# Performance work log

Hardware: AMD Instinct MI355X
Metric: run time of the kernel (lower is better)

## Reference

```python
import jax, jax.numpy as jnp
import numpy as np

B, T, D, H = 4, 2048, 512, 8
DH = D // H  # 64

def setup_inputs() -> dict:
    key = jax.random.key(0)
    kx, kq, kk, kv = jax.random.split(key, 4)
    s = 0.02
    return {
        "x": jax.random.normal(kx, (B, T, D), dtype=jnp.float32),
        "Wq": jax.random.normal(kq, (D, D), dtype=jnp.float32) * s,
        "Wk": jax.random.normal(kk, (D, D), dtype=jnp.float32) * s,
        "Wv": jax.random.normal(kv, (D, D), dtype=jnp.float32) * s,
    }

def reference(x, Wq, Wk, Wv):
    b, t, _ = x.shape
    # nn.Linear(bias=False): y = x @ W.T
    q = (x @ Wq.T).reshape(b, t, H, DH).transpose(0, 2, 1, 3)  # (B,H,T,DH)
    k = (x @ Wk.T).reshape(b, t, H, DH).transpose(0, 2, 1, 3)
    v = (x @ Wv.T).reshape(b, t, H, DH).transpose(0, 2, 1, 3)
    scale = 1.0 / jnp.sqrt(jnp.float32(DH))
    att = jnp.einsum('bhqd,bhkd->bhqk', q, k) * scale  # (B,H,T,T)
    causal = jnp.tril(jnp.ones((t, t), dtype=bool))
    att = jnp.where(causal, att, jnp.float32(-jnp.inf))
    att = jax.nn.softmax(att, axis=-1)
    out = jnp.einsum('bhqk,bhkd->bhqd', att, v)  # (B,H,T,DH)
    return out.transpose(0, 2, 1, 3).reshape(b, t, D)
```

## Files before the change

### kernel.cpp

```cpp
#include <hip/hip_runtime.h>
#include <math.h>

#define B_ 4
#define T_ 2048
#define D_ 512
#define H_ 8
#define DH_ 64

typedef __attribute__((ext_vector_type(8))) short bf16x8;
typedef __attribute__((ext_vector_type(4))) float f32x4;

__device__ inline unsigned short f2b(float x) {
    unsigned int u = __float_as_uint(x);
    return (unsigned short)((u + 0x7FFFu + ((u >> 16) & 1u)) >> 16);
}

__global__ __launch_bounds__(256) void cvt_kernel(
    const float* __restrict__ x,  const float* __restrict__ wq,
    const float* __restrict__ wk, const float* __restrict__ wv,
    unsigned short* __restrict__ xb,  unsigned short* __restrict__ wqb,
    unsigned short* __restrict__ wkb, unsigned short* __restrict__ wvb)
{
    const int bid = blockIdx.x;
    const float* src;
    unsigned short* dst;
    size_t base;
    if (bid < 4096) { src = x; dst = xb; base = (size_t)bid * 1024; }
    else {
        const int s  = (bid - 4096) >> 8;
        const int lb = (bid - 4096) & 255;
        src = (s == 0) ? wq : (s == 1) ? wk : wv;
        dst = (s == 0) ? wqb : (s == 1) ? wkb : wvb;
        base = (size_t)lb * 1024;
    }
    const size_t idx = base + (size_t)threadIdx.x * 4;
    float4 f = *(const float4*)(src + idx);
    ushort4 r;
    r.x = f2b(f.x); r.y = f2b(f.y); r.z = f2b(f.z); r.w = f2b(f.w);
    *(ushort4*)(dst + idx) = r;
}

__global__ __launch_bounds__(256) void qkv_mfma_kernel(
    const unsigned short* __restrict__ xb,
    const unsigned short* __restrict__ wqb,
    const unsigned short* __restrict__ wkb,
    const unsigned short* __restrict__ wvb,
    unsigned short* __restrict__ Qo,
    unsigned short* __restrict__ Ko,
    unsigned short* __restrict__ Vto)
{
    const int z = blockIdx.z;
    const unsigned short* Ap;
    const unsigned short* Bp;
    int m0, n0;
    if (z < 2) {
        Ap = xb; Bp = (z == 0) ? wqb : wkb;
        m0 = blockIdx.x * 128;
        n0 = blockIdx.y * 128;
    } else {
        Ap = wvb; Bp = xb;
        m0 = blockIdx.y * 128;
        n0 = blockIdx.x * 128;
    }
    const int tid = threadIdx.x;
    const int w   = tid >> 6;
    const int l   = tid & 63;
    const int l15 = l & 15;
    const int lg  = l >> 4;
    const int wm  = (w >> 1) * 64;
    const int wn  = (w & 1) * 64;

    __shared__ __align__(16) char lds[32768];
    char* As = lds;
    char* Bs = lds + 16384;

    f32x4 acc[4][4];
    #pragma unroll
    for (int i = 0; i < 4; ++i)
        #pragma unroll
        for (int j = 0; j < 4; ++j) acc[i][j] = (f32x4){0.f, 0.f, 0.f, 0.f};

    bf16x8 areg[4], breg[4];

    #define QLOAD(KS) {                                                        \
        _Pragma("unroll")                                                      \
        for (int i_ = 0; i_ < 4; ++i_) {                                       \
            const int q_ = tid + 256 * i_, r_ = q_ >> 3, c_ = q_ & 7;          \
            areg[i_] = *(const bf16x8*)(Ap + (size_t)(m0 + r_) * 512 + (KS) * 64 + c_ * 8); \
            breg[i_] = *(const bf16x8*)(Bp + (size_t)(n0 + r_) * 512 + (KS) * 64 + c_ * 8); \
        } }

    QLOAD(0);

    for (int ks = 0; ks < 8; ++ks) {
        __syncthreads();
        #pragma unroll
        for (int i = 0; i < 4; ++i) {
            const int q = tid + 256 * i, r = q >> 3, c = q & 7;
            const int off = r * 128 + ((c ^ (r & 7)) << 4);
            *(bf16x8*)(As + off) = areg[i];
            *(bf16x8*)(Bs + off) = breg[i];
        }
        __syncthreads();

        if (ks < 7) QLOAD(ks + 1);

        bf16x8 af[4][2], bf[4][2];
        #pragma unroll
        for (int im = 0; im < 4; ++im) {
            const int r = wm + im * 16 + l15;
            const int rb = r * 128, sw = r & 7;
            af[im][0] = *(const bf16x8*)(As + rb + ((lg ^ sw) << 4));
            af[im][1] = *(const bf16x8*)(As + rb + (((4 + lg) ^ sw) << 4));
        }
        #pragma unroll
        for (int jn = 0; jn < 4; ++jn) {
            const int r = wn + jn * 16 + l15;
            const int rb = r * 128, sw = r & 7;
            bf[jn][0] = *(const bf16x8*)(Bs + rb + ((lg ^ sw) << 4));
            bf[jn][1] = *(const bf16x8*)(Bs + rb + (((4 + lg) ^ sw) << 4));
        }
        #pragma unroll
        for (int im = 0; im < 4; ++im)
            #pragma unroll
            for (int jn = 0; jn < 4; ++jn) {
                acc[im][jn] = __builtin_amdgcn_mfma_f32_16x16x32_bf16(
                    af[im][0], bf[jn][0], acc[im][jn], 0, 0, 0);
                acc[im][jn] = __builtin_amdgcn_mfma_f32_16x16x32_bf16(
                    af[im][1], bf[jn][1], acc[im][jn], 0, 0, 0);
            }
    }

    #undef QLOAD

    if (z < 2) {
        unsigned short* Y = (z == 0) ? Qo : Ko;
        #pragma unroll
        for (int im = 0; im < 4; ++im)
            #pragma unroll
            for (int jn = 0; jn < 4; ++jn)
                #pragma unroll
                for (int r4 = 0; r4 < 4; ++r4) {
                    const int row = m0 + wm + im * 16 + lg * 4 + r4;
                    const int col = n0 + wn + jn * 16 + l15;
                    Y[(size_t)row * 512 + col] = f2b(acc[im][jn][r4]);
                }
    } else {
        #pragma unroll
        for (int im = 0; im < 4; ++im)
            #pragma unroll
            for (int jn = 0; jn < 4; ++jn)
                #pragma unroll
                for (int r4 = 0; r4 < 4; ++r4) {
                    const int rowW = m0 + wm + im * 16 + lg * 4 + r4;
                    const int ct   = n0 + wn + jn * 16 + l15;
                    const int b    = ct >> 11;
                    const int tl   = ct & 2047;
                    Vto[((size_t)(b * 512 + rowW)) * 2048 + tl] = f2b(acc[im][jn][r4]);
                }
    }
}

__global__ __launch_bounds__(256) void attn_mfma_kernel(
    const unsigned short* __restrict__ Q,
    const unsigned short* __restrict__ K,
    const unsigned short* __restrict__ Vt,
    float* __restrict__ O)
{
    const int bid = blockIdx.x;
    const int g   = bid & 31;
    const int h   = g & 7;
    const int b   = g >> 3;
    const int qi  = bid >> 5;
    const int qk_ = qi >> 3, qq_ = qi & 7;
    const int qt  = (qk_ == 0) ? 31 - qq_
                  : (qk_ == 1) ? qq_
                  : (qk_ == 2) ? 23 - qq_
                  :              8 + qq_;
    const int nkt = qt + 1;
    const int tid = threadIdx.x;
    const int w   = tid >> 6;
    const int l   = tid & 63;
    const int l15 = l & 15;
    const int lg  = l >> 4;

    __shared__ __align__(16) char lds[40960];
    char* pw = lds + 32768 + w * 2048;

    const float C  = 0.18033688011112042f;
    const float MC = 32.0f * C;

    const int c0   = tid;
    const int c1   = tid + 256;
    const int row0 = c0 >> 3, seg0 = c0 & 7;
    const int row1 = c1 >> 3, seg1 = c1 & 7;
    const int off0 = row0 * 128 + ((seg0 * 16) ^ ((row0 & 7) << 4));
    const int off1 = row1 * 128 + ((seg1 * 16) ^ ((row1 & 7) << 4));

    const int rowV  = tid >> 2, sp = tid & 3;
    const int kA    = (sp & 1) * 8 + (sp & 2) * 16;
    const int vswz  = (rowV & 7) << 4;
    const int voff0 = rowV * 128 + ((sp * 32) ^ vswz);
    const int voff1 = rowV * 128 + ((sp * 32 + 16) ^ vswz);

    const int t_q      = qt * 64 + w * 16 + l15;
    const size_t qbase = ((size_t)(b * T_ + t_q)) * D_ + h * DH_ + lg * 8;
    const bf16x8 qf0 = *(const bf16x8*)(Q + qbase);
    const bf16x8 qf1 = *(const bf16x8*)(Q + qbase + 32);

    const unsigned short* Ksrc0 = K + ((size_t)(b * T_ + row0)) * D_ + h * DH_ + seg0 * 8;
    const unsigned short* Ksrc1 = K + ((size_t)(b * T_ + row1)) * D_ + h * DH_ + seg1 * 8;
    const unsigned short* VsrcA = Vt + ((size_t)b * D_ + h * DH_ + rowV) * T_ + kA;

    f32x4 o[4];
    #pragma unroll
    for (int d = 0; d < 4; ++d) o[d] = (f32x4){0.f, 0.f, 0.f, 0.f};
    float lrow[4] = {0.f, 0.f, 0.f, 0.f};

    bf16x8 kc0, kc1;
    uint4 va, vb4;

    #define LOADT(KT) {                                                   \
        kc0 = *(const bf16x8*)(Ksrc0 + (size_t)(KT) * (64 * D_));         \
        kc1 = *(const bf16x8*)(Ksrc1 + (size_t)(KT) * (64 * D_));         \
        va  = *(const uint4*)(VsrcA + (KT) * 64);                         \
        vb4 = *(const uint4*)(VsrcA + (KT) * 64 + 16);                    \
    }
    #define WRITEBUF(BI) {                                                \
        char* dK_ = lds + (BI) * 16384;                                   \
        char* dV_ = dK_ + 8192;                                           \
        *(bf16x8*)(dK_ + off0) = kc0;                                     \
        *(bf16x8*)(dK_ + off1) = kc1;                                     \
        uint4 e0_, e1_;                                                   \
        e0_.x = __builtin_amdgcn_perm(vb4.x, va.x, 0x05040100u);          \
        e0_.y = __builtin_amdgcn_perm(vb4.x, va.x, 0x07060302u);          \
        e0_.z = __builtin_amdgcn_perm(vb4.y, va.y, 0x05040100u);          \
        e0_.w = __builtin_amdgcn_perm(vb4.y, va.y, 0x07060302u);          \
        e1_.x = __builtin_amdgcn_perm(vb4.z, va.z, 0x05040100u);          \
        e1_.y = __builtin_amdgcn_perm(vb4.z, va.z, 0x07060302u);          \
        e1_.z = __builtin_amdgcn_perm(vb4.w, va.w, 0x05040100u);          \
        e1_.w = __builtin_amdgcn_perm(vb4.w, va.w, 0x07060302u);          \
        *(uint4*)(dV_ + voff0) = e0_;                                     \
        *(uint4*)(dV_ + voff1) = e1_;                                     \
    }

    LOADT(0);
    WRITEBUF(0);
    if (nkt > 1) LOADT(1);
    __syncthreads();

    for (int kt = 0; kt < nkt; ++kt) {
        char* KsB = lds + (kt & 1) * 16384;
        char* VsB = KsB + 8192;

        if (kt + 1 < nkt) {
            WRITEBUF((kt + 1) & 1);
            if (kt + 2 < nkt) LOADT(kt + 2);
        }

        f32x4 st[4];
        #pragma unroll
        for (int k4 = 0; k4 < 4; ++k4) st[k4] = (f32x4){0.f, 0.f, 0.f, 0.f};
        __builtin_amdgcn_s_setprio(1);
        #pragma unroll
        for (int ktile = 0; ktile < 4; ++ktile) {
            const int krow = ktile * 16 + l15;
            const int rs   = krow * 128;
            const int sw   = (krow & 7) << 4;
            bf16x8 kb0 = *(const bf16x8*)(KsB + rs + ((lg * 16) ^ sw));
            bf16x8 kb1 = *(const bf16x8*)(KsB + rs + ((64 + lg * 16) ^ sw));
            st[ktile] = __builtin_amdgcn_mfma_f32_16x16x32_bf16(qf0, kb0, st[ktile], 0, 0, 0);
            st[ktile] = __builtin_amdgcn_mfma_f32_16x16x32_bf16(qf1, kb1, st[ktile], 0, 0, 0);
        }
        __builtin_amdgcn_s_setprio(0);

        if (kt == qt) {
            const int qloc = w * 16 + lg * 4;
            #pragma unroll
            for (int ktile = 0; ktile < 4; ++ktile) {
                const int key = ktile * 16 + l15;
                #pragma unroll
                for (int r = 0; r < 4; ++r)
                    if (key > qloc + r) st[ktile][r] = -1e30f;
            }
        }

        #pragma unroll
        for (int r = 0; r < 4; ++r) {
            const float p0 = __builtin_amdgcn_exp2f(fmaf(st[0][r], C, -MC));
            const float p1 = __builtin_amdgcn_exp2f(fmaf(st[1][r], C, -MC));
            const float p2 = __builtin_amdgcn_exp2f(fmaf(st[2][r], C, -MC));
            const float p3 = __builtin_amdgcn_exp2f(fmaf(st[3][r], C, -MC));
            lrow[r] += (p0 + p1) + (p2 + p3);
            unsigned pk01, pk23;
            asm("v_cvt_pk_bf16_f32 %0, %1, %2" : "=v"(pk01) : "v"(p0), "v"(p1));
            asm("v_cvt_pk_bf16_f32 %0, %1, %2" : "=v"(pk23) : "v"(p2), "v"(p3));
            const int prow  = lg * 4 + r;
            const int rbase = prow * 128;
            const int swz   = (prow & 7) << 4;
            *(unsigned*)(pw + rbase + ((l15 * 4) ^ swz))      = pk01;
            *(unsigned*)(pw + rbase + ((64 + l15 * 4) ^ swz)) = pk23;
        }

        __builtin_amdgcn_s_setprio(1);
        #pragma unroll
        for (int ks = 0; ks < 2; ++ks) {
            bf16x8 pa = *(const bf16x8*)(pw + l15 * 128 + ((ks * 64 + lg * 16) ^ ((l15 & 7) << 4)));
            #pragma unroll
            for (int d = 0; d < 4; ++d) {
                const int vrow = d * 16 + l15;
                bf16x8 vb = *(const bf16x8*)(VsB + vrow * 128 + ((ks * 64 + lg * 16) ^ ((vrow & 7) << 4)));
                o[d] = __builtin_amdgcn_mfma_f32_16x16x32_bf16(pa, vb, o[d], 0, 0, 0);
            }
        }
        __builtin_amdgcn_s_setprio(0);

        __syncthreads();
    }

    #undef LOADT
    #undef WRITEBUF

    #pragma unroll
    for (int msk = 1; msk <= 8; msk <<= 1)
        #pragma unroll
        for (int r = 0; r < 4; ++r)
            lrow[r] += __shfl_xor(lrow[r], msk);
    float inv[4];
    #pragma unroll
    for (int r = 0; r < 4; ++r) inv[r] = 1.0f / lrow[r];
    #pragma unroll
    for (int d = 0; d < 4; ++d)
        #pragma unroll
        for (int r = 0; r < 4; ++r) {
            const int t = qt * 64 + w * 16 + lg * 4 + r;
            O[((size_t)(b * T_ + t)) * D_ + h * DH_ + d * 16 + l15] = o[d][r] * inv[r];
        }
}

extern "C" void kernel_launch(void* const* d_in, const int* in_sizes, int n_in,
                              void* d_out, int out_size, void* d_ws, size_t ws_size,
                              hipStream_t stream) {
    const float* x  = (const float*)d_in[0];
    const float* Wq = (const float*)d_in[1];
    const float* Wk = (const float*)d_in[2];
    const float* Wv = (const float*)d_in[3];
    float* out = (float*)d_out;

    const size_t xel = (size_t)B_ * T_ * D_;
    const size_t wel = (size_t)D_ * D_;
    unsigned short* xb  = (unsigned short*)d_ws;
    unsigned short* wqb = xb + xel;
    unsigned short* wkb = wqb + wel;
    unsigned short* wvb = wkb + wel;
    unsigned short* Qw  = wvb + wel;
    unsigned short* Kw  = Qw + xel;
    unsigned short* Vtw = Kw + xel;

    cvt_kernel<<<4096 + 3 * 256, 256, 0, stream>>>(x, Wq, Wk, Wv, xb, wqb, wkb, wvb);

    dim3 ggrid(64, 4, 3);
    qkv_mfma_kernel<<<ggrid, 256, 0, stream>>>(xb, wqb, wkb, wvb, Qw, Kw, Vtw);

    attn_mfma_kernel<<<1024, 256, 0, stream>>>(Qw, Kw, Vtw, out);
}
```

Baseline: 64.89 us.

## Compute S transposed so P stays in registers for PV MFMA

The QK^T MFMA operands are swapped so each lane holds scores for one query across 16 keys. The bf16-packed probabilities can then feed the PV MFMA directly as A operands, with no LDS round trip for P. The V-tile staging drops the byte-permute interleave and changes the key offset mapping to match the new K ordering, and LDS shrinks by 8KB. Row sums become a single per-lane value reduced across lane groups, then redistributed with shuffles before the final normalisation.

```diff
diff --git a/kernel.cpp b/kernel.cpp
--- a/kernel.cpp
+++ b/kernel.cpp
@@ -9,10 +9,17 @@
 
 typedef __attribute__((ext_vector_type(8))) short bf16x8;
 typedef __attribute__((ext_vector_type(4))) float f32x4;
+typedef __attribute__((ext_vector_type(4))) unsigned u32x4;
 
 __device__ inline unsigned short f2b(float x) {
     unsigned int u = __float_as_uint(x);
     return (unsigned short)((u + 0x7FFFu + ((u >> 16) & 1u)) >> 16);
+}
+
+__device__ inline unsigned cvtpk(float a, float b) {
+    unsigned r;
+    asm("v_cvt_pk_bf16_f32 %0, %1, %2" : "=v"(r) : "v"(a), "v"(b));
+    return r;
 }
 
 __global__ __launch_bounds__(256) void cvt_kernel(
@@ -184,8 +191,7 @@
     const int l15 = l & 15;
     const int lg  = l >> 4;
 
-    __shared__ __align__(16) char lds[40960];
-    char* pw = lds + 32768 + w * 2048;
+    __shared__ __align__(16) char lds[32768];
 
     const float C  = 0.18033688011112042f;
     const float MC = 32.0f * C;
@@ -198,7 +204,7 @@
     const int off1 = row1 * 128 + ((seg1 * 16) ^ ((row1 & 7) << 4));
 
     const int rowV  = tid >> 2, sp = tid & 3;
-    const int kA    = (sp & 1) * 8 + (sp & 2) * 16;
+    const int kA    = (sp >> 1) * 32 + (sp & 1) * 8;
     const int vswz  = (rowV & 7) << 4;
     const int voff0 = rowV * 128 + ((sp * 32) ^ vswz);
     const int voff1 = rowV * 128 + ((sp * 32 + 16) ^ vswz);
@@ -215,7 +221,7 @@
     f32x4 o[4];
     #pragma unroll
     for (int d = 0; d < 4; ++d) o[d] = (f32x4){0.f, 0.f, 0.f, 0.f};
-    float lrow[4] = {0.f, 0.f, 0.f, 0.f};
+    float lrow = 0.f;
 
     bf16x8 kc0, kc1;
     uint4 va, vb4;
@@ -232,14 +238,8 @@
         *(bf16x8*)(dK_ + off0) = kc0;                                     \
         *(bf16x8*)(dK_ + off1) = kc1;                                     \
         uint4 e0_, e1_;                                                   \
-        e0_.x = __builtin_amdgcn_perm(vb4.x, va.x, 0x05040100u);          \
-        e0_.y = __builtin_amdgcn_perm(vb4.x, va.x, 0x07060302u);          \
-        e0_.z = __builtin_amdgcn_perm(vb4.y, va.y, 0x05040100u);          \
-        e0_.w = __builtin_amdgcn_perm(vb4.y, va.y, 0x07060302u);          \
-        e1_.x = __builtin_amdgcn_perm(vb4.z, va.z, 0x05040100u);          \
-        e1_.y = __builtin_amdgcn_perm(vb4.z, va.z, 0x07060302u);          \
-        e1_.z = __builtin_amdgcn_perm(vb4.w, va.w, 0x05040100u);          \
-        e1_.w = __builtin_amdgcn_perm(vb4.w, va.w, 0x07060302u);          \
+        e0_.x = va.x;  e0_.y = va.y;  e0_.z = vb4.x; e0_.w = vb4.y;       \
+        e1_.x = va.z;  e1_.y = va.w;  e1_.z = vb4.z; e1_.w = vb4.w;       \
         *(uint4*)(dV_ + voff0) = e0_;                                     \
         *(uint4*)(dV_ + voff1) = e1_;                                     \
     }
@@ -269,49 +269,54 @@
             const int sw   = (krow & 7) << 4;
             bf16x8 kb0 = *(const bf16x8*)(KsB + rs + ((lg * 16) ^ sw));
             bf16x8 kb1 = *(const bf16x8*)(KsB + rs + ((64 + lg * 16) ^ sw));
-            st[ktile] = __builtin_amdgcn_mfma_f32_16x16x32_bf16(qf0, kb0, st[ktile], 0, 0, 0);
-            st[ktile] = __builtin_amdgcn_mfma_f32_16x16x32_bf16(qf1, kb1, st[ktile], 0, 0, 0);
+            st[ktile] = __builtin_amdgcn_mfma_f32_16x16x32_bf16(kb0, qf0, st[ktile], 0, 0, 0);
+            st[ktile] = __builtin_amdgcn_mfma_f32_16x16x32_bf16(kb1, qf1, st[ktile], 0, 0, 0);
         }
         __builtin_amdgcn_s_setprio(0);
 
         if (kt == qt) {
-            const int qloc = w * 16 + lg * 4;
+            const int qloc = w * 16 + l15;
             #pragma unroll
             for (int ktile = 0; ktile < 4; ++ktile) {
-                const int key = ktile * 16 + l15;
                 #pragma unroll
-                for (int r = 0; r < 4; ++r)
-                    if (key > qloc + r) st[ktile][r] = -1e30f;
+                for (int r = 0; r < 4; ++r) {
+                    const int key = ktile * 16 + lg * 4 + r;
+                    if (key > qloc) st[ktile][r] = -1e30f;
+                }
             }
         }
 
-        #pragma unroll
-        for (int r = 0; r < 4; ++r) {
-            const float p0 = __builtin_amdgcn_exp2f(fmaf(st[0][r], C, -MC));
-            const float p1 = __builtin_amdgcn_exp2f(fmaf(st[1][r], C, -MC));
-            const float p2 = __builtin_amdgcn_exp2f(fmaf(st[2][r], C, -MC));
-            const float p3 = __builtin_amdgcn_exp2f(fmaf(st[3][r], C, -MC));
-            lrow[r] += (p0 + p1) + (p2 + p3);
-            unsigned pk01, pk23;
-            asm("v_cvt_pk_bf16_f32 %0, %1, %2" : "=v"(pk01) : "v"(p0), "v"(p1));
-            asm("v_cvt_pk_bf16_f32 %0, %1, %2" : "=v"(pk23) : "v"(p2), "v"(p3));
-            const int prow  = lg * 4 + r;
-            const int rbase = prow * 128;
-            const int swz   = (prow & 7) << 4;
-            *(unsigned*)(pw + rbase + ((l15 * 4) ^ swz))      = pk01;
-            *(unsigned*)(pw + rbase + ((64 + l15 * 4) ^ swz)) = pk23;
-        }
+        float p[4][4];
+        #pragma unroll
+        for (int t = 0; t < 4; ++t) {
+            #pragma unroll
+            for (int r = 0; r < 4; ++r)
+                p[t][r] = __builtin_amdgcn_exp2f(fmaf(st[t][r], C, -MC));
+            lrow += (p[t][0] + p[t][1]) + (p[t][2] + p[t][3]);
+        }
+        const unsigned pw0 = cvtpk(p[0][0], p[0][1]);
+        const unsigned pw1 = cvtpk(p[0][2], p[0][3]);
+        const unsigned pw2 = cvtpk(p[1][0], p[1][1]);
+        const unsigned pw3 = cvtpk(p[1][2], p[1][3]);
+        const unsigned pw4 = cvtpk(p[2][0], p[2][1]);
+        const unsigned pw5 = cvtpk(p[2][2], p[2][3]);
+        const unsigned pw6 = cvtpk(p[3][0], p[3][1]);
+        const unsigned pw7 = cvtpk(p[3][2], p[3][3]);
+        const u32x4 aw0 = {pw0, pw1, pw2, pw3};
+        const u32x4 aw1 = {pw4, pw5, pw6, pw7};
+        const bf16x8 pa0 = __builtin_bit_cast(bf16x8, aw0);
+        const bf16x8 pa1 = __builtin_bit_cast(bf16x8, aw1);
 
         __builtin_amdgcn_s_setprio(1);
         #pragma unroll
-        for (int ks = 0; ks < 2; ++ks) {
-            bf16x8 pa = *(const bf16x8*)(pw + l15 * 128 + ((ks * 64 + lg * 16) ^ ((l15 & 7) << 4)));
-            #pragma unroll
-            for (int d = 0; d < 4; ++d) {
-                const int vrow = d * 16 + l15;
-                bf16x8 vb = *(const bf16x8*)(VsB + vrow * 128 + ((ks * 64 + lg * 16) ^ ((vrow & 7) << 4)));
-                o[d] = __builtin_amdgcn_mfma_f32_16x16x32_bf16(pa, vb, o[d], 0, 0, 0);
-            }
+        for (int d = 0; d < 4; ++d) {
+            const int vrow = d * 16 + l15;
+            const int rb   = vrow * 128;
+            const int sw   = (vrow & 7) << 4;
+            bf16x8 vb0 = *(const bf16x8*)(VsB + rb + ((lg * 16) ^ sw));
+            bf16x8 vb1 = *(const bf16x8*)(VsB + rb + ((64 + lg * 16) ^ sw));
+            o[d] = __builtin_amdgcn_mfma_f32_16x16x32_bf16(pa0, vb0, o[d], 0, 0, 0);
+            o[d] = __builtin_amdgcn_mfma_f32_16x16x32_bf16(pa1, vb1, o[d], 0, 0, 0);
         }
         __builtin_amdgcn_s_setprio(0);
 
@@ -321,20 +326,18 @@
     #undef LOADT
     #undef WRITEBUF
 
+    lrow += __shfl_xor(lrow, 16);
+    lrow += __shfl_xor(lrow, 32);
+    const float inv = 1.0f / lrow;
+    float invr[4];
     #pragma unroll
-    for (int msk = 1; msk <= 8; msk <<= 1)
-        #pragma unroll
-        for (int r = 0; r < 4; ++r)
-            lrow[r] += __shfl_xor(lrow[r], msk);
-    float inv[4];
-    #pragma unroll
-    for (int r = 0; r < 4; ++r) inv[r] = 1.0f / lrow[r];
+    for (int r = 0; r < 4; ++r) invr[r] = __shfl(inv, lg * 4 + r);
     #pragma unroll
     for (int d = 0; d < 4; ++d)
         #pragma unroll
         for (int r = 0; r < 4; ++r) {
             const int t = qt * 64 + w * 16 + lg * 4 + r;
-            O[((size_t)(b * T_ + t)) * D_ + h * DH_ + d * 16 + l15] = o[d][r] * inv[r];
+            O[((size_t)(b * T_ + t)) * D_ + h * DH_ + d * 16 + l15] = o[d][r] * invr[r];
         }
 }
 
```

Measured after the change: 68.32 us. 1.05x slower.

## Use 128-row query tiles with 512 threads sharing K/V loads in attention

Applied to the files above, without the earlier changes.

Each attention block now covers 128 query rows with 8 waves instead of 64 rows with 4, so every K/V tile staged in LDS serves twice as many queries and global K/V traffic per query roughly halves. The load work is split so half the threads load K and half load V. Waves in the lower half skip compute on the last key tile but still join every barrier. Launching half as many blocks with a coarser causal schedule may leave work less evenly spread across CUs, and LDS use per block grows.

```diff
diff --git a/kernel.cpp b/kernel.cpp
--- a/kernel.cpp
+++ b/kernel.cpp
@@ -161,7 +161,7 @@
     }
 }
 
-__global__ __launch_bounds__(256) void attn_mfma_kernel(
+__global__ __launch_bounds__(512) void attn_mfma_kernel(
     const unsigned short* __restrict__ Q,
     const unsigned short* __restrict__ K,
     const unsigned short* __restrict__ Vt,
@@ -172,44 +172,43 @@
     const int h   = g & 7;
     const int b   = g >> 3;
     const int qi  = bid >> 5;
-    const int qk_ = qi >> 3, qq_ = qi & 7;
-    const int qt  = (qk_ == 0) ? 31 - qq_
-                  : (qk_ == 1) ? qq_
-                  : (qk_ == 2) ? 23 - qq_
-                  :              8 + qq_;
-    const int nkt = qt + 1;
+    const int qt  = (qi < 8) ? (15 - qi) : (qi - 8);
+    const int nkt = 2 * qt + 2;
     const int tid = threadIdx.x;
     const int w   = tid >> 6;
+    const int wl  = w & 3;
+    const int wh  = w >> 2;
     const int l   = tid & 63;
     const int l15 = l & 15;
     const int lg  = l >> 4;
 
-    __shared__ __align__(16) char lds[40960];
+    __shared__ __align__(16) char lds[49152];
     char* pw = lds + 32768 + w * 2048;
 
     const float C  = 0.18033688011112042f;
     const float MC = 32.0f * C;
 
-    const int c0   = tid;
-    const int c1   = tid + 256;
-    const int row0 = c0 >> 3, seg0 = c0 & 7;
-    const int row1 = c1 >> 3, seg1 = c1 & 7;
+    const bool isK = (tid >= 256);
+    const int  t2  = tid & 255;
+
+    const int row0 = t2 >> 3, seg0 = t2 & 7;
+    const int row1 = row0 + 32;
     const int off0 = row0 * 128 + ((seg0 * 16) ^ ((row0 & 7) << 4));
-    const int off1 = row1 * 128 + ((seg1 * 16) ^ ((row1 & 7) << 4));
-
-    const int rowV  = tid >> 2, sp = tid & 3;
+    const int off1 = row1 * 128 + ((seg0 * 16) ^ ((row1 & 7) << 4));
+
+    const int rowV  = t2 >> 2, sp = t2 & 3;
     const int kA    = (sp & 1) * 8 + (sp & 2) * 16;
     const int vswz  = (rowV & 7) << 4;
     const int voff0 = rowV * 128 + ((sp * 32) ^ vswz);
     const int voff1 = rowV * 128 + ((sp * 32 + 16) ^ vswz);
 
-    const int t_q      = qt * 64 + w * 16 + l15;
+    const int t_q      = qt * 128 + wh * 64 + wl * 16 + l15;
     const size_t qbase = ((size_t)(b * T_ + t_q)) * D_ + h * DH_ + lg * 8;
     const bf16x8 qf0 = *(const bf16x8*)(Q + qbase);
     const bf16x8 qf1 = *(const bf16x8*)(Q + qbase + 32);
 
     const unsigned short* Ksrc0 = K + ((size_t)(b * T_ + row0)) * D_ + h * DH_ + seg0 * 8;
-    const unsigned short* Ksrc1 = K + ((size_t)(b * T_ + row1)) * D_ + h * DH_ + seg1 * 8;
+    const unsigned short* Ksrc1 = K + ((size_t)(b * T_ + row1)) * D_ + h * DH_ + seg0 * 8;
     const unsigned short* VsrcA = Vt + ((size_t)b * D_ + h * DH_ + rowV) * T_ + kA;
 
     f32x4 o[4];
@@ -221,33 +220,39 @@
     uint4 va, vb4;
 
     #define LOADT(KT) {                                                   \
-        kc0 = *(const bf16x8*)(Ksrc0 + (size_t)(KT) * (64 * D_));         \
-        kc1 = *(const bf16x8*)(Ksrc1 + (size_t)(KT) * (64 * D_));         \
-        va  = *(const uint4*)(VsrcA + (KT) * 64);                         \
-        vb4 = *(const uint4*)(VsrcA + (KT) * 64 + 16);                    \
-    }
+        if (isK) {                                                        \
+            kc0 = *(const bf16x8*)(Ksrc0 + (size_t)(KT) * (64 * D_));     \
+            kc1 = *(const bf16x8*)(Ksrc1 + (size_t)(KT) * (64 * D_));     \
+        } else {                                                          \
+            va  = *(const uint4*)(VsrcA + (KT) * 64);                     \
+            vb4 = *(const uint4*)(VsrcA + (KT) * 64 + 16);                \
+        } }
     #define WRITEBUF(BI) {                                                \
         char* dK_ = lds + (BI) * 16384;                                   \
         char* dV_ = dK_ + 8192;                                           \
-        *(bf16x8*)(dK_ + off0) = kc0;                                     \
-        *(bf16x8*)(dK_ + off1) = kc1;                                     \
-        uint4 e0_, e1_;                                                   \
-        e0_.x = __builtin_amdgcn_perm(vb4.x, va.x, 0x05040100u);          \
-        e0_.y = __builtin_amdgcn_perm(vb4.x, va.x, 0x07060302u);          \
-        e0_.z = __builtin_amdgcn_perm(vb4.y, va.y, 0x05040100u);          \
-        e0_.w = __builtin_amdgcn_perm(vb4.y, va.y, 0x07060302u);          \
-        e1_.x = __builtin_amdgcn_perm(vb4.z, va.z, 0x05040100u);          \
-        e1_.y = __builtin_amdgcn_perm(vb4.z, va.z, 0x07060302u);          \
-        e1_.z = __builtin_amdgcn_perm(vb4.w, va.w, 0x05040100u);          \
-        e1_.w = __builtin_amdgcn_perm(vb4.w, va.w, 0x07060302u);          \
-        *(uint4*)(dV_ + voff0) = e0_;                                     \
-        *(uint4*)(dV_ + voff1) = e1_;                                     \
-    }
+        if (isK) {                                                        \
+            *(bf16x8*)(dK_ + off0) = kc0;                                 \
+            *(bf16x8*)(dK_ + off1) = kc1;                                 \
+        } else {                                                          \
+            uint4 e0_, e1_;                                               \
+            e0_.x = __builtin_amdgcn_perm(vb4.x, va.x, 0x05040100u);      \
+            e0_.y = __builtin_amdgcn_perm(vb4.x, va.x, 0x07060302u);      \
+            e0_.z = __builtin_amdgcn_perm(vb4.y, va.y, 0x05040100u);      \
+            e0_.w = __builtin_amdgcn_perm(vb4.y, va.y, 0x07060302u);      \
+            e1_.x = __builtin_amdgcn_perm(vb4.z, va.z, 0x05040100u);      \
+            e1_.y = __builtin_amdgcn_perm(vb4.z, va.z, 0x07060302u);      \
+            e1_.z = __builtin_amdgcn_perm(vb4.w, va.w, 0x05040100u);      \
+            e1_.w = __builtin_amdgcn_perm(vb4.w, va.w, 0x07060302u);      \
+            *(uint4*)(dV_ + voff0) = e0_;                                 \
+            *(uint4*)(dV_ + voff1) = e1_;                                 \
+        } }
 
     LOADT(0);
     WRITEBUF(0);
-    if (nkt > 1) LOADT(1);
+    LOADT(1);
     __syncthreads();
+
+    const int dia = 2 * qt + wh;
 
     for (int kt = 0; kt < nkt; ++kt) {
         char* KsB = lds + (kt & 1) * 16384;
@@ -258,62 +263,64 @@
             if (kt + 2 < nkt) LOADT(kt + 2);
         }
 
-        f32x4 st[4];
-        #pragma unroll
-        for (int k4 = 0; k4 < 4; ++k4) st[k4] = (f32x4){0.f, 0.f, 0.f, 0.f};
-        __builtin_amdgcn_s_setprio(1);
-        #pragma unroll
-        for (int ktile = 0; ktile < 4; ++ktile) {
-            const int krow = ktile * 16 + l15;
-            const int rs   = krow * 128;
-            const int sw   = (krow & 7) << 4;
-            bf16x8 kb0 = *(const bf16x8*)(KsB + rs + ((lg * 16) ^ sw));
-            bf16x8 kb1 = *(const bf16x8*)(KsB + rs + ((64 + lg * 16) ^ sw));
-            st[ktile] = __builtin_amdgcn_mfma_f32_16x16x32_bf16(qf0, kb0, st[ktile], 0, 0, 0);
-            st[ktile] = __builtin_amdgcn_mfma_f32_16x16x32_bf16(qf1, kb1, st[ktile], 0, 0, 0);
-        }
-        __builtin_amdgcn_s_setprio(0);
-
-        if (kt == qt) {
-            const int qloc = w * 16 + lg * 4;
+        if (kt <= dia) {
+            f32x4 st[4];
+            #pragma unroll
+            for (int k4 = 0; k4 < 4; ++k4) st[k4] = (f32x4){0.f, 0.f, 0.f, 0.f};
+            __builtin_amdgcn_s_setprio(1);
             #pragma unroll
             for (int ktile = 0; ktile < 4; ++ktile) {
-                const int key = ktile * 16 + l15;
+                const int krow = ktile * 16 + l15;
+                const int rs   = krow * 128;
+                const int sw   = (krow & 7) << 4;
+                bf16x8 kb0 = *(const bf16x8*)(KsB + rs + ((lg * 16) ^ sw));
+                bf16x8 kb1 = *(const bf16x8*)(KsB + rs + ((64 + lg * 16) ^ sw));
+                st[ktile] = __builtin_amdgcn_mfma_f32_16x16x32_bf16(qf0, kb0, st[ktile], 0, 0, 0);
+                st[ktile] = __builtin_amdgcn_mfma_f32_16x16x32_bf16(qf1, kb1, st[ktile], 0, 0, 0);
+            }
+            __builtin_amdgcn_s_setprio(0);
+
+            if (kt == dia) {
+                const int qloc = wl * 16 + lg * 4;
                 #pragma unroll
-                for (int r = 0; r < 4; ++r)
-                    if (key > qloc + r) st[ktile][r] = -1e30f;
-            }
-        }
-
-        #pragma unroll
-        for (int r = 0; r < 4; ++r) {
-            const float p0 = __builtin_amdgcn_exp2f(fmaf(st[0][r], C, -MC));
-            const float p1 = __builtin_amdgcn_exp2f(fmaf(st[1][r], C, -MC));
-            const float p2 = __builtin_amdgcn_exp2f(fmaf(st[2][r], C, -MC));
-            const float p3 = __builtin_amdgcn_exp2f(fmaf(st[3][r], C, -MC));
-            lrow[r] += (p0 + p1) + (p2 + p3);
-            unsigned pk01, pk23;
-            asm("v_cvt_pk_bf16_f32 %0, %1, %2" : "=v"(pk01) : "v"(p0), "v"(p1));
-            asm("v_cvt_pk_bf16_f32 %0, %1, %2" : "=v"(pk23) : "v"(p2), "v"(p3));
-            const int prow  = lg * 4 + r;
-            const int rbase = prow * 128;
-            const int swz   = (prow & 7) << 4;
-            *(unsigned*)(pw + rbase + ((l15 * 4) ^ swz))      = pk01;
-            *(unsigned*)(pw + rbase + ((64 + l15 * 4) ^ swz)) = pk23;
-        }
-
-        __builtin_amdgcn_s_setprio(1);
-        #pragma unroll
-        for (int ks = 0; ks < 2; ++ks) {
-            bf16x8 pa = *(const bf16x8*)(pw + l15 * 128 + ((ks * 64 + lg * 16) ^ ((l15 & 7) << 4)));
-            #pragma unroll
-            for (int d = 0; d < 4; ++d) {
-                const int vrow = d * 16 + l15;
-                bf16x8 vb = *(const bf16x8*)(VsB + vrow * 128 + ((ks * 64 + lg * 16) ^ ((vrow & 7) << 4)));
-                o[d] = __builtin_amdgcn_mfma_f32_16x16x32_bf16(pa, vb, o[d], 0, 0, 0);
-            }
-        }
-        __builtin_amdgcn_s_setprio(0);
+                for (int ktile = 0; ktile < 4; ++ktile) {
+                    const int key = ktile * 16 + l15;
+                    #pragma unroll
+                    for (int r = 0; r < 4; ++r)
+                        if (key > qloc + r) st[ktile][r] = -1e30f;
+                }
+            }
+
+            #pragma unroll
+            for (int r = 0; r < 4; ++r) {
+                const float p0 = __builtin_amdgcn_exp2f(fmaf(st[0][r], C, -MC));
+                const float p1 = __builtin_amdgcn_exp2f(fmaf(st[1][r], C, -MC));
+                const float p2 = __builtin_amdgcn_exp2f(fmaf(st[2][r], C, -MC));
+                const float p3 = __builtin_amdgcn_exp2f(fmaf(st[3][r], C, -MC));
+                lrow[r] += (p0 + p1) + (p2 + p3);
+                unsigned pk01, pk23;
+                asm("v_cvt_pk_bf16_f32 %0, %1, %2" : "=v"(pk01) : "v"(p0), "v"(p1));
+                asm("v_cvt_pk_bf16_f32 %0, %1, %2" : "=v"(pk23) : "v"(p2), "v"(p3));
+                const int prow  = lg * 4 + r;
+                const int rbase = prow * 128;
+                const int swz   = (prow & 7) << 4;
+                *(unsigned*)(pw + rbase + ((l15 * 4) ^ swz))      = pk01;
+                *(unsigned*)(pw + rbase + ((64 + l15 * 4) ^ swz)) = pk23;
+            }
+
+            __builtin_amdgcn_s_setprio(1);
+            #pragma unroll
+            for (int ks = 0; ks < 2; ++ks) {
+                bf16x8 pa = *(const bf16x8*)(pw + l15 * 128 + ((ks * 64 + lg * 16) ^ ((l15 & 7) << 4)));
+                #pragma unroll
+                for (int d = 0; d < 4; ++d) {
+                    const int vrow = d * 16 + l15;
+                    bf16x8 vb = *(const bf16x8*)(VsB + vrow * 128 + ((ks * 64 + lg * 16) ^ ((vrow & 7) << 4)));
+                    o[d] = __builtin_amdgcn_mfma_f32_16x16x32_bf16(pa, vb, o[d], 0, 0, 0);
+                }
+            }
+            __builtin_amdgcn_s_setprio(0);
+        }
 
         __syncthreads();
     }
@@ -333,7 +340,7 @@
     for (int d = 0; d < 4; ++d)
         #pragma unroll
         for (int r = 0; r < 4; ++r) {
-            const int t = qt * 64 + w * 16 + lg * 4 + r;
+            const int t = qt * 128 + wh * 64 + wl * 16 + lg * 4 + r;
             O[((size_t)(b * T_ + t)) * D_ + h * DH_ + d * 16 + l15] = o[d][r] * inv[r];
         }
 }
@@ -362,5 +369,5 @@
     dim3 ggrid(64, 4, 3);
     qkv_mfma_kernel<<<ggrid, 256, 0, stream>>>(xb, wqb, wkb, wvb, Qw, Kw, Vtw);
 
-    attn_mfma_kernel<<<1024, 256, 0, stream>>>(Qw, Kw, Vtw, out);
-}
+    attn_mfma_kernel<<<512, 512, 0, stream>>>(Qw, Kw, Vtw, out);
+}
```

Measured after the change: 73.90 us. +13.9%, slower.
